# Kernel optimization log

Measured on AMD Instinct MI355X. Metric: run time of the kernel, lower is better.

## Reference

```python
import jax, jax.numpy as jnp
import numpy as np
from jax import lax

B, T, D_IN = 512, 128, 512
HID, C = 256, 96
MAX_LEN = 25  # num_steps = MAX_LEN + 1


def setup_inputs() -> dict:
    key = jax.random.key(0)
    ks = jax.random.split(key, 12)
    num_steps = MAX_LEN + 1
    gru_in = D_IN + C
    inp = {
        "batch_H": jax.random.normal(ks[0], (B, T, D_IN), dtype=jnp.float32),
        "text": jax.random.randint(ks[1], (B, num_steps), 0, C, dtype=jnp.int64),
        "batch_max_length": MAX_LEN,
        # attention params
        "W_i2h": jax.random.normal(ks[2], (HID, D_IN), dtype=jnp.float32) * 0.04,
        "W_h2h": jax.random.normal(ks[3], (HID, HID), dtype=jnp.float32) * 0.06,
        "b_h2h": jnp.zeros((HID,), dtype=jnp.float32),
        "W_score": jax.random.normal(ks[4], (1, HID), dtype=jnp.float32) * 0.08,
        # GRUCell params (torch layout: [3H, in], gate order r, z, n)
        "W_ih": jax.random.normal(ks[5], (3 * HID, gru_in), dtype=jnp.float32) * 0.04,
        "W_hh": jax.random.normal(ks[6], (3 * HID, HID), dtype=jnp.float32) * 0.06,
        "b_ih": jnp.zeros((3 * HID,), dtype=jnp.float32),
        "b_hh": jnp.zeros((3 * HID,), dtype=jnp.float32),
        # generator
        "W_gen": jax.random.normal(ks[7], (C, HID), dtype=jnp.float32) * 0.07,
        "b_gen": jnp.zeros((C,), dtype=jnp.float32),
    }
    return inp


def reference(batch_H, text, batch_max_length, W_i2h, W_h2h, b_h2h, W_score,
              W_ih, W_hh, b_ih, b_hh, W_gen, b_gen):
    num_steps = batch_max_length + 1
    hid = W_h2h.shape[0]
    n_cls = W_gen.shape[0]
    dtype = batch_H.dtype
    bsz = batch_H.shape[0]

    # i2h(batch_H) is loop-invariant: [B, T, H]
    H_proj = jnp.einsum("btd,hd->bth", batch_H, W_i2h)

    def step(hidden, char_ids):
        # additive attention
        h_proj = hidden @ W_h2h.T + b_h2h                      # [B, H]
        e = jnp.tanh(H_proj + h_proj[:, None, :]) @ W_score[0]  # [B, T]
        alpha = jax.nn.softmax(e, axis=1)                       # [B, T]
        context = jnp.einsum("bt,btd->bd", alpha, batch_H)      # [B, D]
        onehot = jax.nn.one_hot(char_ids, n_cls, dtype=dtype)
        x = jnp.concatenate([context, onehot], axis=1)
        # GRUCell (torch semantics)
        gi = x @ W_ih.T + b_ih
        gh = hidden @ W_hh.T + b_hh
        i_r, i_z, i_n = jnp.split(gi, 3, axis=1)
        h_r, h_z, h_n = jnp.split(gh, 3, axis=1)
        r = jax.nn.sigmoid(i_r + h_r)
        z = jax.nn.sigmoid(i_z + h_z)
        n = jnp.tanh(i_n + r * h_n)
        new_h = (1.0 - z) * n + z * hidden
        return new_h, new_h

    h0 = jnp.zeros((bsz, hid), dtype=dtype)
    chars = jnp.swapaxes(text[:, :num_steps], 0, 1)  # [num_steps, B]
    _, hiddens = lax.scan(step, h0, chars)           # [num_steps, B, H]
    hiddens = jnp.swapaxes(hiddens, 0, 1)            # [B, num_steps, H]
    probs = hiddens @ W_gen.T + b_gen                # [B, num_steps, C]
    return probs
```

## Files before the change

kernel.cpp:

```cpp
#include <hip/hip_runtime.h>

#define BATCH 512
#define TLEN 128
#define DIN 512
#define HID 256
#define NCLS 96
#define STEPS 26
#define GRUIN 608
#define G3 768

#define BM 64
#define BN 64
#define BK 16
#define LDS_STRIDE 68

typedef unsigned short ushort_t;
typedef __attribute__((ext_vector_type(8))) short short8v;
typedef __attribute__((ext_vector_type(4))) float f32x4;
typedef __attribute__((ext_vector_type(8))) unsigned short ushort8v;

__device__ __forceinline__ float fast_tanh(float x) {
    return 1.f - 2.f / (__expf(2.f * x) + 1.f);
}
__device__ __forceinline__ float fast_sigmoid(float x) {
    return 1.f / (1.f + __expf(-x));
}
__device__ __forceinline__ ushort_t f2bf_rne(float f) {
    unsigned int u = __float_as_uint(f);
    unsigned int r = (u + 0x7FFFu + ((u >> 16) & 1u)) >> 16;
    return (ushort_t)r;
}
__device__ __forceinline__ float bf2f(ushort_t h) {
    return __uint_as_float(((unsigned int)h) << 16);
}

__global__ __launch_bounds__(256)
void prep_all(const float* __restrict__ W_h2h, const float* __restrict__ W_hh,
              const float* __restrict__ W_ih, const float* __restrict__ W_i2h,
              const float* __restrict__ b_ih, const float* __restrict__ b_h2h,
              const float* __restrict__ b_hh, const float* __restrict__ W_gen,
              ushort_t* __restrict__ Wcat16, ushort_t* __restrict__ B16cat,
              float* __restrict__ WembT, ushort_t* __restrict__ Wgen16,
              float* __restrict__ bcat, float* __restrict__ hidden,
              float* __restrict__ hg) {
    int idx = blockIdx.x * 256 + threadIdx.x;
    if (idx < 262144) {
        int n = idx >> 8, k = idx & 255;
        float v = (n < 256) ? W_h2h[n * 256 + k] : W_hh[(size_t)(n - 256) * 256 + k];
        Wcat16[idx] = f2bf_rne(v);
    } else if (idx < 262144 + 524288) {
        int j = idx - 262144;
        int r = j >> 9, c = j & 511;
        float v = (r < 768) ? W_ih[(size_t)r * GRUIN + c] : W_i2h[(size_t)(r - 768) * 512 + c];
        B16cat[j] = f2bf_rne(v);
    } else if (idx < 262144 + 524288 + 73728) {
        int j = idx - (262144 + 524288);
        int ch = j / 768, jj = j - ch * 768;
        WembT[j] = W_ih[(size_t)jj * GRUIN + 512 + ch] + b_ih[jj];
    } else if (idx < 262144 + 524288 + 73728 + 24576) {
        int j = idx - (262144 + 524288 + 73728);
        Wgen16[j] = f2bf_rne(W_gen[j]);
    } else if (idx < 262144 + 524288 + 73728 + 24576 + 1024) {
        int j = idx - (262144 + 524288 + 73728 + 24576);
        bcat[j] = (j < 256) ? b_h2h[j] : b_hh[j - 256];
    } else if (idx < 262144 + 524288 + 73728 + 24576 + 1024 + 131072) {
        int j = idx - (262144 + 524288 + 73728 + 24576 + 1024);
        hidden[j] = 0.f;
    } else if (idx < 262144 + 524288 + 73728 + 24576 + 1024 + 131072 + 524288) {
        int j = idx - (262144 + 524288 + 73728 + 24576 + 1024 + 131072);
        int c = j & 1023;
        hg[j] = (c < 256) ? b_h2h[c] : b_hh[c - 256];
    }
}

__global__ __launch_bounds__(256)
void conv_a16(const float* __restrict__ src, ushort_t* __restrict__ dst, int n8) {
    int i = blockIdx.x * 256 + threadIdx.x;
    const int stride = gridDim.x * 256;
    for (; i < n8; i += stride) {
        float4 v0 = ((const float4*)src)[2 * i];
        float4 v1 = ((const float4*)src)[2 * i + 1];
        ushort8v o;
        o[0] = f2bf_rne(v0.x); o[1] = f2bf_rne(v0.y);
        o[2] = f2bf_rne(v0.z); o[3] = f2bf_rne(v0.w);
        o[4] = f2bf_rne(v1.x); o[5] = f2bf_rne(v1.y);
        o[6] = f2bf_rne(v1.z); o[7] = f2bf_rne(v1.w);
        ((ushort8v*)dst)[i] = o;
    }
}

__device__ __forceinline__ int swz(int row, int col8) {
    return (row * 32 + col8 * 8) ^ ((row & 7) << 3);
}

__global__ __launch_bounds__(256)
void hwhp_mfma(const ushort_t* __restrict__ A16,
               const ushort_t* __restrict__ B16,
               ushort_t* __restrict__ HW16,
               ushort_t* __restrict__ Hp16) {
    __shared__ ushort_t As[128 * 32];
    __shared__ ushort_t Bs[128 * 32];
    const int wgid = blockIdx.x;
    const int mt = (wgid & 7) + ((wgid >> 6) << 3);
    const int nt = (wgid >> 3) & 7;
    const int bm = mt * 128, bn = nt * 128;
    const int tid = threadIdx.x;
    const int wid = tid >> 6, lane = tid & 63;
    const int wr = wid >> 1, wc = wid & 1;
    const int sr = tid >> 2, sq = tid & 3;
    f32x4 acc[4][4] = {};
    const int l15 = lane & 15, lhi = lane >> 4;
    for (int k0 = 0; k0 < 512; k0 += 32) {
        ushort8v a0 = *(const ushort8v*)(A16 + (size_t)(bm + sr) * 512 + k0 + sq * 8);
        ushort8v a1 = *(const ushort8v*)(A16 + (size_t)(bm + sr + 64) * 512 + k0 + sq * 8);
        ushort8v b0 = *(const ushort8v*)(B16 + (size_t)(bn + sr) * 512 + k0 + sq * 8);
        ushort8v b1 = *(const ushort8v*)(B16 + (size_t)(bn + sr + 64) * 512 + k0 + sq * 8);
        __syncthreads();
        *(ushort8v*)(&As[swz(sr, sq)]) = a0;
        *(ushort8v*)(&As[swz(sr + 64, sq)]) = a1;
        *(ushort8v*)(&Bs[swz(sr, sq)]) = b0;
        *(ushort8v*)(&Bs[swz(sr + 64, sq)]) = b1;
        __syncthreads();
        short8v af[4], bfr[4];
#pragma unroll
        for (int i = 0; i < 4; ++i) {
            int arow = wr * 64 + i * 16 + l15;
            af[i] = *(const short8v*)(&As[swz(arow, lhi)]);
            int brow = wc * 64 + i * 16 + l15;
            bfr[i] = *(const short8v*)(&Bs[swz(brow, lhi)]);
        }
#pragma unroll
        for (int i = 0; i < 4; ++i)
#pragma unroll
            for (int j = 0; j < 4; ++j)
                acc[i][j] = __builtin_amdgcn_mfma_f32_16x16x32_bf16(af[i], bfr[j], acc[i][j], 0, 0, 0);
    }
    const int cr0 = bm + wr * 64 + lhi * 4;
    const int cc0 = bn + wc * 64 + l15;
    const bool isHW = (bn < 768);
    ushort_t* outp = isHW ? HW16 : Hp16;
    const int ld = isHW ? 768 : 256;
    const int coff = isHW ? 0 : 768;
#pragma unroll
    for (int i = 0; i < 4; ++i)
#pragma unroll
        for (int j = 0; j < 4; ++j)
#pragma unroll
            for (int p = 0; p < 4; ++p)
                outp[(size_t)(cr0 + i * 16 + p) * ld + (cc0 + j * 16 - coff)] = f2bf_rne(acc[i][j][p]);
}

__global__ __launch_bounds__(256)
void hg_mfma(const ushort_t* __restrict__ H16,
             const ushort_t* __restrict__ W16,
             const float* __restrict__ bcat,
             float* __restrict__ hg) {
    __shared__ ushort_t As[128 * 32];
    __shared__ ushort_t Bs[128 * 32];
    const int wgid = blockIdx.x;
    const int mt = wgid >> 3;
    const int nt = wgid & 7;
    const int bm = mt * 128, bn = nt * 128;
    const int tid = threadIdx.x;
    const int wid = tid >> 6, lane = tid & 63;
    const int wr = wid >> 1, wc = wid & 1;
    const int sr = tid >> 2, sq = tid & 3;
    f32x4 acc[4][4] = {};
    const int l15 = lane & 15, lhi = lane >> 4;
    for (int k0 = 0; k0 < 256; k0 += 32) {
        ushort8v a0 = *(const ushort8v*)(H16 + (size_t)(bm + sr) * 256 + k0 + sq * 8);
        ushort8v a1 = *(const ushort8v*)(H16 + (size_t)(bm + sr + 64) * 256 + k0 + sq * 8);
        ushort8v b0 = *(const ushort8v*)(W16 + (size_t)(bn + sr) * 256 + k0 + sq * 8);
        ushort8v b1 = *(const ushort8v*)(W16 + (size_t)(bn + sr + 64) * 256 + k0 + sq * 8);
        __syncthreads();
        *(ushort8v*)(&As[swz(sr, sq)]) = a0;
        *(ushort8v*)(&As[swz(sr + 64, sq)]) = a1;
        *(ushort8v*)(&Bs[swz(sr, sq)]) = b0;
        *(ushort8v*)(&Bs[swz(sr + 64, sq)]) = b1;
        __syncthreads();
        short8v af[4], bfr[4];
#pragma unroll
        for (int i = 0; i < 4; ++i) {
            int arow = wr * 64 + i * 16 + l15;
            af[i] = *(const short8v*)(&As[swz(arow, lhi)]);
            int brow = wc * 64 + i * 16 + l15;
            bfr[i] = *(const short8v*)(&Bs[swz(brow, lhi)]);
        }
#pragma unroll
        for (int i = 0; i < 4; ++i)
#pragma unroll
            for (int j = 0; j < 4; ++j)
                acc[i][j] = __builtin_amdgcn_mfma_f32_16x16x32_bf16(af[i], bfr[j], acc[i][j], 0, 0, 0);
    }
    const int cr0 = bm + wr * 64 + lhi * 4;
    const int cc0 = bn + wc * 64 + l15;
#pragma unroll
    for (int j = 0; j < 4; ++j) {
        const int c = cc0 + j * 16;
        const float bj = bcat[c];
#pragma unroll
        for (int i = 0; i < 4; ++i)
#pragma unroll
            for (int p = 0; p < 4; ++p)
                hg[(size_t)(cr0 + i * 16 + p) * 1024 + c] = acc[i][j][p] + bj;
    }
}

__global__ __launch_bounds__(1024, 8)
void step_fused(const ushort_t* __restrict__ HW16,
                const ushort_t* __restrict__ Hp16,
                const float* __restrict__ hg,
                const float* __restrict__ WembT,
                const ushort_t* __restrict__ Wgen16,
                const float* __restrict__ Wscore,
                const float* __restrict__ b_gen,
                const int* __restrict__ text,
                int s,
                float* __restrict__ hidden,
                ushort_t* __restrict__ hidden16,
                float* __restrict__ out) {
    const int b = blockIdx.x;
    const int tid = threadIdx.x;
    const int wave = tid >> 6, lane = tid & 63;

    __shared__ __align__(16) float hp[HID];
    __shared__ __align__(16) float wsc[HID];
    __shared__ __align__(16) float parts[6144];
    __shared__ __align__(16) float gi_l[G3];
    __shared__ __align__(16) float sh[HID];
    __shared__ float es[TLEN];
    __shared__ float al[TLEN];
    __shared__ float red[16];

    const size_t rowbase = (size_t)b * TLEN;
    if (tid < 256) {
        hp[tid] = hg[(size_t)b * 1024 + tid];
        wsc[tid] = Wscore[tid];
    }
    __syncthreads();

#pragma unroll
    for (int i = 0; i < 8; ++i) {
        int t = i * 16 + wave;
        ushort4 hv = *(const ushort4*)(Hp16 + (rowbase + t) * 256 + lane * 4);
        float4 hpv = *(const float4*)(&hp[lane * 4]);
        float4 wv = *(const float4*)(&wsc[lane * 4]);
        float sc = fast_tanh(bf2f(hv.x) + hpv.x) * wv.x
                 + fast_tanh(bf2f(hv.y) + hpv.y) * wv.y
                 + fast_tanh(bf2f(hv.z) + hpv.z) * wv.z
                 + fast_tanh(bf2f(hv.w) + hpv.w) * wv.w;
#pragma unroll
        for (int off = 32; off >= 1; off >>= 1) sc += __shfl_xor(sc, off);
        if (lane == 0) es[t] = sc;
    }
    __syncthreads();
    float ev = 0.f, p = 0.f;
    if (tid < TLEN) {
        ev = es[tid];
        float mx = ev;
#pragma unroll
        for (int off = 32; off >= 1; off >>= 1) mx = fmaxf(mx, __shfl_xor(mx, off));
        if (lane == 0) red[wave] = mx;
    }
    __syncthreads();
    if (tid < TLEN) {
        float m = fmaxf(red[0], red[1]);
        p = __expf(ev - m);
        float sm = p;
#pragma unroll
        for (int off = 32; off >= 1; off >>= 1) sm += __shfl_xor(sm, off);
        if (lane == 0) red[8 + wave] = sm;
    }
    __syncthreads();
    if (tid < TLEN) al[tid] = p / (red[8] + red[9]);
    __syncthreads();
    {
        const int tg = tid >> 7;
        const int cq = tid & 127;
        if (cq < 96) {
            float a0 = 0.f, a1 = 0.f, a2 = 0.f, a3 = 0.f;
            float a4 = 0.f, a5 = 0.f, a6 = 0.f, a7 = 0.f;
            const ushort_t* base = HW16 + (rowbase + tg * 16) * 768 + cq * 8;
            const float* alh = &al[tg * 16];
#pragma unroll 4
            for (int i = 0; i < 16; ++i) {
                ushort8v v = *(const ushort8v*)(base + (size_t)i * 768);
                float a = alh[i];
                a0 = fmaf(a, bf2f(v[0]), a0);
                a1 = fmaf(a, bf2f(v[1]), a1);
                a2 = fmaf(a, bf2f(v[2]), a2);
                a3 = fmaf(a, bf2f(v[3]), a3);
                a4 = fmaf(a, bf2f(v[4]), a4);
                a5 = fmaf(a, bf2f(v[5]), a5);
                a6 = fmaf(a, bf2f(v[6]), a6);
                a7 = fmaf(a, bf2f(v[7]), a7);
            }
            float* pr = &parts[tg * 768 + cq * 8];
            pr[0] = a0; pr[1] = a1; pr[2] = a2; pr[3] = a3;
            pr[4] = a4; pr[5] = a5; pr[6] = a6; pr[7] = a7;
        }
    }
    __syncthreads();
    if (tid < G3) {
        float g = parts[tid] + parts[768 + tid] + parts[1536 + tid] + parts[2304 + tid]
                + parts[3072 + tid] + parts[3840 + tid] + parts[4608 + tid] + parts[5376 + tid];
        gi_l[tid] = g;
    }
    __syncthreads();
    if (tid < 256) {
        const int ch = text[b * STEPS + s];
        const float* em = WembT + (size_t)ch * G3;
        const float* ghb = hg + (size_t)b * 1024 + 256;
        float ir = gi_l[tid]       + em[tid]       + ghb[tid];
        float iz = gi_l[256 + tid] + em[256 + tid] + ghb[256 + tid];
        float in_ = gi_l[512 + tid] + em[512 + tid];
        float hn = ghb[512 + tid];
        float rr = fast_sigmoid(ir);
        float zz = fast_sigmoid(iz);
        float nn = fast_tanh(in_ + rr * hn);
        float nh = (1.f - zz) * nn + zz * hidden[(size_t)b * HID + tid];
        hidden[(size_t)b * HID + tid] = nh;
        hidden16[(size_t)b * HID + tid] = f2bf_rne(nh);
        sh[tid] = nh;
    }
    __syncthreads();
    if (tid < NCLS) {
        const ushort_t* wrow = Wgen16 + (size_t)tid * HID;
        float acc = b_gen[tid];
#pragma unroll 4
        for (int k = 0; k < HID; k += 8) {
            ushort8v w8 = *(const ushort8v*)(wrow + k);
            acc = fmaf(sh[k],     bf2f(w8[0]), acc);
            acc = fmaf(sh[k + 1], bf2f(w8[1]), acc);
            acc = fmaf(sh[k + 2], bf2f(w8[2]), acc);
            acc = fmaf(sh[k + 3], bf2f(w8[3]), acc);
            acc = fmaf(sh[k + 4], bf2f(w8[4]), acc);
            acc = fmaf(sh[k + 5], bf2f(w8[5]), acc);
            acc = fmaf(sh[k + 6], bf2f(w8[6]), acc);
            acc = fmaf(sh[k + 7], bf2f(w8[7]), acc);
        }
        out[((size_t)b * STEPS + s) * NCLS + tid] = acc;
    }
}

template <typename OutT>
__device__ __forceinline__ void store_c(OutT* p, float v);
template <> __device__ __forceinline__ void store_c<float>(float* p, float v) { *p = v; }
template <> __device__ __forceinline__ void store_c<ushort_t>(ushort_t* p, float v) { *p = f2bf_rne(v); }

template <typename OutT>
__global__ __launch_bounds__(256)
void gemm_nt(const float* __restrict__ A, int lda,
             const float* __restrict__ Bw, int ldb,
             OutT* __restrict__ Cc, int ldc,
             const float* __restrict__ bias,
             int M, int N, int K) {
    __shared__ float As[BK][LDS_STRIDE];
    __shared__ float Bs[BK][LDS_STRIDE];
    const int tid = threadIdx.x;
    const int bm = blockIdx.x * BM;
    const int bn = blockIdx.y * BN;
    const int tx = tid & 15, ty = tid >> 4;
    const int lr = tid >> 2;
    const int lc = (tid & 3) << 2;
    float acc[4][4] = {};
    const int gr = bm + lr;
    const int gn = bn + lr;
    const float* Arow = A + (size_t)gr * lda;
    const float* Brow = Bw + (size_t)gn * ldb;
    for (int k0 = 0; k0 < K; k0 += BK) {
        float4 va = make_float4(0.f, 0.f, 0.f, 0.f);
        float4 vb = make_float4(0.f, 0.f, 0.f, 0.f);
        if (gr < M) va = *(const float4*)(Arow + k0 + lc);
        if (gn < N) vb = *(const float4*)(Brow + k0 + lc);
        As[lc + 0][lr] = va.x; As[lc + 1][lr] = va.y;
        As[lc + 2][lr] = va.z; As[lc + 3][lr] = va.w;
        Bs[lc + 0][lr] = vb.x; Bs[lc + 1][lr] = vb.y;
        Bs[lc + 2][lr] = vb.z; Bs[lc + 3][lr] = vb.w;
        __syncthreads();
#pragma unroll
        for (int k = 0; k < BK; ++k) {
            float4 a4 = *(const float4*)(&As[k][ty << 2]);
            float4 b4 = *(const float4*)(&Bs[k][tx << 2]);
            float a[4] = {a4.x, a4.y, a4.z, a4.w};
            float b[4] = {b4.x, b4.y, b4.z, b4.w};
#pragma unroll
            for (int i = 0; i < 4; ++i)
#pragma unroll
                for (int j = 0; j < 4; ++j)
                    acc[i][j] = fmaf(a[i], b[j], acc[i][j]);
        }
        __syncthreads();
    }
#pragma unroll
    for (int i = 0; i < 4; ++i) {
        int m = bm + (ty << 2) + i;
        if (m >= M) continue;
#pragma unroll
        for (int j = 0; j < 4; ++j) {
            int n = bn + (tx << 2) + j;
            if (n < N) store_c(&Cc[(size_t)m * ldc + n], acc[i][j] + (bias ? bias[n] : 0.f));
        }
    }
}

__global__ __launch_bounds__(256)
void prep_wcat(const float* __restrict__ W_h2h, const float* __restrict__ W_hh,
               const float* __restrict__ b_h2h, const float* __restrict__ b_hh,
               float* __restrict__ Wcat, float* __restrict__ bcat,
               float* __restrict__ hidden) {
    int idx = blockIdx.x * 256 + threadIdx.x;
    int r = idx >> 8, c = idx & 255;
    Wcat[idx] = (r < 256) ? W_h2h[r * 256 + c] : W_hh[(r - 256) * 256 + c];
    if (idx < 1024) bcat[idx] = (idx < 256) ? b_h2h[idx] : b_hh[idx - 256];
    if (idx < BATCH * HID) hidden[idx] = 0.f;
}

template <typename HT>
__global__ __launch_bounds__(256)
void attn_step(const HT* __restrict__ Hproj,
               const float* __restrict__ batchH,
               const float* __restrict__ hg,
               const float* __restrict__ Wscore,
               float* __restrict__ context) {
    const int b = blockIdx.x;
    const int tid = threadIdx.x;
    __shared__ float hp[HID];
    __shared__ float wsc[HID];
    __shared__ float es[TLEN];
    __shared__ float red[16];
    hp[tid] = hg[b * 1024 + tid];
    wsc[tid] = Wscore[tid];
    __syncthreads();
    const int wave = tid >> 6;
    const int lane = tid & 63;
    const HT* Hp = Hproj + (size_t)b * TLEN * HID;
    for (int t = wave; t < TLEN; t += 4) {
        float x0, x1, x2, x3;
        if constexpr (sizeof(HT) == 4) {
            float4 hv = *(const float4*)((const float*)Hp + (size_t)t * HID + (lane << 2));
            x0 = hv.x; x1 = hv.y; x2 = hv.z; x3 = hv.w;
        } else {
            ushort4 hv = *(const ushort4*)((const ushort_t*)Hp + (size_t)t * HID + (lane << 2));
            x0 = bf2f(hv.x); x1 = bf2f(hv.y); x2 = bf2f(hv.z); x3 = bf2f(hv.w);
        }
        float4 hpv = *(const float4*)(&hp[lane << 2]);
        float4 wv = *(const float4*)(&wsc[lane << 2]);
        float sc = fast_tanh(x0 + hpv.x) * wv.x
                 + fast_tanh(x1 + hpv.y) * wv.y
                 + fast_tanh(x2 + hpv.z) * wv.z
                 + fast_tanh(x3 + hpv.w) * wv.w;
#pragma unroll
        for (int off = 32; off >= 1; off >>= 1) sc += __shfl_xor(sc, off);
        if (lane == 0) es[t] = sc;
    }
    __syncthreads();
    float e = (tid < TLEN) ? es[tid] : -INFINITY;
    float m = e;
#pragma unroll
    for (int off = 32; off >= 1; off >>= 1) m = fmaxf(m, __shfl_xor(m, off));
    if (lane == 0) red[wave] = m;
    __syncthreads();
    m = fmaxf(fmaxf(red[0], red[1]), fmaxf(red[2], red[3]));
    float p = (tid < TLEN) ? __expf(e - m) : 0.f;
    float ss = p;
#pragma unroll
    for (int off = 32; off >= 1; off >>= 1) ss += __shfl_xor(ss, off);
    if (lane == 0) red[8 + wave] = ss;
    __syncthreads();
    float denom = red[8] + red[9] + red[10] + red[11];
    if (tid < TLEN) es[tid] = p / denom;
    __syncthreads();
    const float* Hb = batchH + (size_t)b * TLEN * DIN;
    float acc0 = 0.f, acc1 = 0.f;
#pragma unroll 4
    for (int t = 0; t < TLEN; ++t) {
        float a = es[t];
        acc0 = fmaf(a, Hb[(size_t)t * DIN + tid], acc0);
        acc1 = fmaf(a, Hb[(size_t)t * DIN + HID + tid], acc1);
    }
    context[(size_t)b * DIN + tid] = acc0;
    context[(size_t)b * DIN + HID + tid] = acc1;
}

__global__ __launch_bounds__(256)
void gru_gate_gen(const float* __restrict__ gi,
                  const float* __restrict__ hg,
                  float* __restrict__ hidden,
                  float* __restrict__ out,
                  const int* __restrict__ text,
                  int s,
                  const float* __restrict__ W_ih,
                  const float* __restrict__ W_gen,
                  const float* __restrict__ b_gen) {
    const int b = blockIdx.x;
    const int h = threadIdx.x;
    __shared__ float sh[HID];
    const int ch = text[b * STEPS + s];
    const float* gib = gi + (size_t)b * G3;
    const float* ghb = hg + (size_t)b * 1024 + 256;
    float ir = gib[h]        + W_ih[(size_t)h * GRUIN + DIN + ch];
    float iz = gib[256 + h]  + W_ih[(size_t)(256 + h) * GRUIN + DIN + ch];
    float in_ = gib[512 + h] + W_ih[(size_t)(512 + h) * GRUIN + DIN + ch];
    float hr = ghb[h];
    float hz = ghb[256 + h];
    float hn = ghb[512 + h];
    float r = fast_sigmoid(ir + hr);
    float z = fast_sigmoid(iz + hz);
    float n = fast_tanh(in_ + r * hn);
    float hprev = hidden[b * HID + h];
    float nh = (1.f - z) * n + z * hprev;
    hidden[b * HID + h] = nh;
    sh[h] = nh;
    __syncthreads();
    if (h < NCLS) {
        const float* wg = W_gen + (size_t)h * HID;
        float acc = b_gen[h];
#pragma unroll 4
        for (int k = 0; k < HID; k += 4) {
            float4 w4 = *(const float4*)(wg + k);
            acc = fmaf(sh[k], w4.x, acc);
            acc = fmaf(sh[k + 1], w4.y, acc);
            acc = fmaf(sh[k + 2], w4.z, acc);
            acc = fmaf(sh[k + 3], w4.w, acc);
        }
        out[((size_t)b * STEPS + s) * NCLS + h] = acc;
    }
}

extern "C" void kernel_launch(void* const* d_in, const int* in_sizes, int n_in,
                              void* d_out, int out_size, void* d_ws, size_t ws_size,
                              hipStream_t stream) {
    const float* batch_H = (const float*)d_in[0];
    const int* text      = (const int*)d_in[1];
    const float* W_i2h   = (const float*)d_in[3];
    const float* W_h2h   = (const float*)d_in[4];
    const float* b_h2h   = (const float*)d_in[5];
    const float* W_score = (const float*)d_in[6];
    const float* W_ih    = (const float*)d_in[7];
    const float* W_hh    = (const float*)d_in[8];
    const float* b_ih    = (const float*)d_in[9];
    const float* b_hh    = (const float*)d_in[10];
    const float* W_gen   = (const float*)d_in[11];
    const float* b_gen   = (const float*)d_in[12];
    float* out = (float*)d_out;
    char* ws = (char*)d_ws;

    const size_t M = (size_t)BATCH * TLEN;
    const size_t nBH = M * DIN;
    const size_t hw_off     = 0;
    const size_t hp_off     = 100663296;
    const size_t a16_off    = hp_off + 33554432;
    const size_t b16cat_off = a16_off + 67108864;
    const size_t wcat_off   = b16cat_off + 1048576;
    const size_t wembT_off  = wcat_off + 524288;
    const size_t wgen16_off = wembT_off + 294912;
    const size_t bcat_off   = wgen16_off + 49152;
    const size_t hg_off     = bcat_off + 4096;
    const size_t hidden_off = hg_off + 2097152;
    const size_t h16_off    = hidden_off + 524288;
    const size_t need_new   = h16_off + 262144;

    if (ws_size >= need_new) {
        ushort_t* HW16     = (ushort_t*)(ws + hw_off);
        ushort_t* Hp16     = (ushort_t*)(ws + hp_off);
        ushort_t* A16      = (ushort_t*)(ws + a16_off);
        ushort_t* B16cat   = (ushort_t*)(ws + b16cat_off);
        ushort_t* Wcat16   = (ushort_t*)(ws + wcat_off);
        float*    WembT    = (float*)(ws + wembT_off);
        ushort_t* Wgen16   = (ushort_t*)(ws + wgen16_off);
        float*    bcat     = (float*)(ws + bcat_off);
        float*    hg       = (float*)(ws + hg_off);
        float*    hidden   = (float*)(ws + hidden_off);
        ushort_t* hidden16 = (ushort_t*)(ws + h16_off);

        hipLaunchKernelGGL(prep_all, dim3(6020), dim3(256), 0, stream,
                           W_h2h, W_hh, W_ih, W_i2h, b_ih, b_h2h, b_hh, W_gen,
                           Wcat16, B16cat, WembT, Wgen16, bcat, hidden, hg);
        hipLaunchKernelGGL(conv_a16, dim3(2048), dim3(256), 0, stream,
                           batch_H, A16, (int)(nBH / 8));
        hipLaunchKernelGGL(hwhp_mfma, dim3((M / 128) * 8), dim3(256), 0, stream,
                           A16, B16cat, HW16, Hp16);
        for (int s = 0; s < STEPS; ++s) {
            hipLaunchKernelGGL(step_fused, dim3(BATCH), dim3(1024), 0, stream,
                               HW16, Hp16, hg, WembT, Wgen16, W_score,
                               b_gen, text, s, hidden, hidden16, out);
            if (s < STEPS - 1) {
                hipLaunchKernelGGL(hg_mfma, dim3(32), dim3(256), 0, stream,
                                   hidden16, Wcat16, bcat, hg);
            }
        }
        return;
    }

    const size_t nHp = M * HID;
    const size_t small_floats = (size_t)BATCH * HID + BATCH * 1024 + BATCH * DIN
                              + BATCH * G3 + 1024 * HID + 1024;
    const size_t need_B32 = nHp * 4 + small_floats * 4;
    const bool use_fp32 = (ws_size >= need_B32);
    const size_t hp_bytes = use_fp32 ? nHp * 4 : nHp * 2;
    void* Hproj = (void*)ws;
    float* hiddenB = (float*)(ws + hp_bytes);
    float* hgB     = hiddenB + BATCH * HID;
    float* context = hgB + BATCH * 1024;
    float* gi      = context + BATCH * DIN;
    float* Wcat    = gi + BATCH * G3;
    float* bcatB   = Wcat + 1024 * HID;

    hipLaunchKernelGGL(prep_wcat, dim3(1024), dim3(256), 0, stream,
                       W_h2h, W_hh, b_h2h, b_hh, Wcat, bcatB, hiddenB);
    if (use_fp32) {
        hipLaunchKernelGGL(gemm_nt<float>, dim3(M / BM, HID / BN), dim3(256), 0, stream,
                           batch_H, DIN, W_i2h, DIN, (float*)Hproj, HID, (const float*)nullptr,
                           (int)M, HID, DIN);
    } else {
        hipLaunchKernelGGL(gemm_nt<ushort_t>, dim3(M / BM, HID / BN), dim3(256), 0, stream,
                           batch_H, DIN, W_i2h, DIN, (ushort_t*)Hproj, HID, (const float*)nullptr,
                           (int)M, HID, DIN);
    }
    for (int s = 0; s < STEPS; ++s) {
        hipLaunchKernelGGL(gemm_nt<float>, dim3(BATCH / BM, 1024 / BN), dim3(256), 0, stream,
                           hiddenB, HID, Wcat, HID, hgB, 1024, bcatB, BATCH, 1024, HID);
        if (use_fp32) {
            hipLaunchKernelGGL(attn_step<float>, dim3(BATCH), dim3(256), 0, stream,
                               (const float*)Hproj, batch_H, hgB, W_score, context);
        } else {
            hipLaunchKernelGGL(attn_step<ushort_t>, dim3(BATCH), dim3(256), 0, stream,
                               (const ushort_t*)Hproj, batch_H, hgB, W_score, context);
        }
        hipLaunchKernelGGL(gemm_nt<float>, dim3(BATCH / BM, G3 / BN), dim3(256), 0, stream,
                           context, DIN, W_ih, GRUIN, gi, G3, b_ih, BATCH, G3, DIN);
        hipLaunchKernelGGL(gru_gate_gen, dim3(BATCH), dim3(HID), 0, stream,
                           gi, hgB, hiddenB, out, text, s, W_ih, W_gen, b_gen);
    }
}
```

Measured before the change: 1.072 ms.

## Use direct global-to-LDS loads in hwhp GEMM and halve hg_mfma M-tile

```diff
diff --git a/kernel.cpp b/kernel.cpp
--- a/kernel.cpp
+++ b/kernel.cpp
@@ -107,19 +107,25 @@
     const int tid = threadIdx.x;
     const int wid = tid >> 6, lane = tid & 63;
     const int wr = wid >> 1, wc = wid & 1;
-    const int sr = tid >> 2, sq = tid & 3;
     f32x4 acc[4][4] = {};
     const int l15 = lane & 15, lhi = lane >> 4;
+    const int rin = (lane >> 2) ^ ((lane >> 4) & 1);
+    const int qsrc = (lane & 3) ^ (rin & 3);
     for (int k0 = 0; k0 < 512; k0 += 32) {
-        ushort8v a0 = *(const ushort8v*)(A16 + (size_t)(bm + sr) * 512 + k0 + sq * 8);
-        ushort8v a1 = *(const ushort8v*)(A16 + (size_t)(bm + sr + 64) * 512 + k0 + sq * 8);
-        ushort8v b0 = *(const ushort8v*)(B16 + (size_t)(bn + sr) * 512 + k0 + sq * 8);
-        ushort8v b1 = *(const ushort8v*)(B16 + (size_t)(bn + sr + 64) * 512 + k0 + sq * 8);
         __syncthreads();
-        *(ushort8v*)(&As[swz(sr, sq)]) = a0;
-        *(ushort8v*)(&As[swz(sr + 64, sq)]) = a1;
-        *(ushort8v*)(&Bs[swz(sr, sq)]) = b0;
-        *(ushort8v*)(&Bs[swz(sr + 64, sq)]) = b1;
+#pragma unroll
+        for (int c = 0; c < 2; ++c) {
+            const int chunk = wid + 4 * c;
+            const int row = chunk * 16 + rin;
+            __builtin_amdgcn_global_load_lds(
+                (const __attribute__((address_space(1))) void*)(A16 + (size_t)(bm + row) * 512 + k0 + qsrc * 8),
+                (__attribute__((address_space(3))) void*)(As + chunk * 512),
+                16, 0, 0);
+            __builtin_amdgcn_global_load_lds(
+                (const __attribute__((address_space(1))) void*)(B16 + (size_t)(bn + row) * 512 + k0 + qsrc * 8),
+                (__attribute__((address_space(3))) void*)(Bs + chunk * 512),
+                16, 0, 0);
+        }
         __syncthreads();
         short8v af[4], bfr[4];
 #pragma unroll
@@ -155,51 +161,52 @@
              const ushort_t* __restrict__ W16,
              const float* __restrict__ bcat,
              float* __restrict__ hg) {
-    __shared__ ushort_t As[128 * 32];
+    __shared__ ushort_t As[64 * 32];
     __shared__ ushort_t Bs[128 * 32];
     const int wgid = blockIdx.x;
     const int mt = wgid >> 3;
     const int nt = wgid & 7;
-    const int bm = mt * 128, bn = nt * 128;
+    const int bm = mt * 64, bn = nt * 128;
     const int tid = threadIdx.x;
     const int wid = tid >> 6, lane = tid & 63;
     const int wr = wid >> 1, wc = wid & 1;
     const int sr = tid >> 2, sq = tid & 3;
-    f32x4 acc[4][4] = {};
+    f32x4 acc[2][4] = {};
     const int l15 = lane & 15, lhi = lane >> 4;
     for (int k0 = 0; k0 < 256; k0 += 32) {
-        ushort8v a0 = *(const ushort8v*)(H16 + (size_t)(bm + sr) * 256 + k0 + sq * 8);
-        ushort8v a1 = *(const ushort8v*)(H16 + (size_t)(bm + sr + 64) * 256 + k0 + sq * 8);
+        ushort8v a0 = *(const ushort8v*)(H16 + (size_t)(bm + (sr & 63)) * 256 + k0 + sq * 8);
         ushort8v b0 = *(const ushort8v*)(W16 + (size_t)(bn + sr) * 256 + k0 + sq * 8);
         ushort8v b1 = *(const ushort8v*)(W16 + (size_t)(bn + sr + 64) * 256 + k0 + sq * 8);
         __syncthreads();
-        *(ushort8v*)(&As[swz(sr, sq)]) = a0;
-        *(ushort8v*)(&As[swz(sr + 64, sq)]) = a1;
+        if (sr < 64) *(ushort8v*)(&As[swz(sr, sq)]) = a0;
         *(ushort8v*)(&Bs[swz(sr, sq)]) = b0;
         *(ushort8v*)(&Bs[swz(sr + 64, sq)]) = b1;
         __syncthreads();
-        short8v af[4], bfr[4];
-#pragma unroll
-        for (int i = 0; i < 4; ++i) {
-            int arow = wr * 64 + i * 16 + l15;
+        short8v af[2], bfr[4];
+#pragma unroll
+        for (int i = 0; i < 2; ++i) {
+            int arow = wr * 32 + i * 16 + l15;
             af[i] = *(const short8v*)(&As[swz(arow, lhi)]);
-            int brow = wc * 64 + i * 16 + l15;
-            bfr[i] = *(const short8v*)(&Bs[swz(brow, lhi)]);
-        }
-#pragma unroll
-        for (int i = 0; i < 4; ++i)
+        }
+#pragma unroll
+        for (int j = 0; j < 4; ++j) {
+            int brow = wc * 64 + j * 16 + l15;
+            bfr[j] = *(const short8v*)(&Bs[swz(brow, lhi)]);
+        }
+#pragma unroll
+        for (int i = 0; i < 2; ++i)
 #pragma unroll
             for (int j = 0; j < 4; ++j)
                 acc[i][j] = __builtin_amdgcn_mfma_f32_16x16x32_bf16(af[i], bfr[j], acc[i][j], 0, 0, 0);
     }
-    const int cr0 = bm + wr * 64 + lhi * 4;
+    const int cr0 = bm + wr * 32 + lhi * 4;
     const int cc0 = bn + wc * 64 + l15;
 #pragma unroll
     for (int j = 0; j < 4; ++j) {
         const int c = cc0 + j * 16;
         const float bj = bcat[c];
 #pragma unroll
-        for (int i = 0; i < 4; ++i)
+        for (int i = 0; i < 2; ++i)
 #pragma unroll
             for (int p = 0; p < 4; ++p)
                 hg[(size_t)(cr0 + i * 16 + p) * 1024 + c] = acc[i][j][p] + bj;
@@ -586,7 +593,7 @@
                                HW16, Hp16, hg, WembT, Wgen16, W_score,
                                b_gen, text, s, hidden, hidden16, out);
             if (s < STEPS - 1) {
-                hipLaunchKernelGGL(hg_mfma, dim3(32), dim3(256), 0, stream,
+                hipLaunchKernelGGL(hg_mfma, dim3(64), dim3(256), 0, stream,
                                    hidden16, Wcat16, bcat, hg);
             }
         }
```

Measured after the change: 1.031 ms. -3.9%, faster.
